# Performance work log

Measured on AMD Instinct MI355X. Metric: run time of the kernel, lower is better.

Reference implementation:

```python
import jax, jax.numpy as jnp
import numpy as np


def setup_inputs() -> dict:
    key = jax.random.key(0)
    k1, k2 = jax.random.split(key)
    N, D, G = 200000, 256, 512
    x = jax.random.normal(k1, (N, D), dtype=jnp.float32)
    batch_ids = jnp.sort(jax.random.randint(k2, (N,), 0, G, dtype=jnp.int64))
    return {"x": x, "batch_ids": batch_ids, "num_graphs": G}


def reference(x, batch_ids, num_graphs):
    # Segment-mean: equivalent to the per-graph masked mean loop.
    sums = jax.ops.segment_sum(x, batch_ids, num_segments=num_graphs)  # [G, D]
    counts = jax.ops.segment_sum(jnp.ones((x.shape[0],), dtype=x.dtype),
                                 batch_ids, num_segments=num_graphs)  # [G]
    graph_features = sums / counts[:, None]
    return graph_features
```

## Files before the change

kernel.cpp:

```cpp
#include <hip/hip_runtime.h>


#define SPLIT 4

__global__ __launch_bounds__(256) void segmean_partial(
    const float* __restrict__ x,
    const int*   __restrict__ ids,
    float*       __restrict__ part,
    int*         __restrict__ cnts,
    int N, int D, int G)
{
    const int bid = (int)blockIdx.x;
    const int g   = bid >> 2;
    const int q   = bid & 3;

    const int W  = 4096;
    const int v0 = g, v1 = g + 1;
    const long long c0 = (long long)v0 * N / G;
    const long long c1 = (long long)v1 * N / G;
    int lo0 = (int)(c0 - W < 0 ? 0 : c0 - W);
    int hi0 = (int)(c0 + W > N ? N : c0 + W);
    int lo1 = (int)(c1 - W < 0 ? 0 : c1 - W);
    int hi1 = (int)(c1 + W > N ? N : c1 + W);
    const bool ok0 = (lo0 == 0 || ids[lo0 - 1] < v0) && (hi0 == N || ids[hi0] >= v0);
    const bool ok1 = (lo1 == 0 || ids[lo1 - 1] < v1) && (hi1 == N || ids[hi1] >= v1);
    if (!ok0) { lo0 = 0; hi0 = N; }
    if (!ok1) { lo1 = 0; hi1 = N; }
    while ((lo0 < hi0) | (lo1 < hi1)) {
        if (lo0 < hi0) {
            const int m = (lo0 + hi0) >> 1;
            if (ids[m] < v0) lo0 = m + 1; else hi0 = m;
        }
        if (lo1 < hi1) {
            const int m = (lo1 + hi1) >> 1;
            if (ids[m] < v1) lo1 = m + 1; else hi1 = m;
        }
    }
    const int start = lo0, end = lo1;
    const int count = end - start;

    const int chunk = (count + SPLIT - 1) >> 2;
    const int r0 = start + q * chunk;
    const int r1 = (r0 + chunk < end) ? (r0 + chunk) : end;

    const int t      = (int)threadIdx.x;
    const int rowoff = t >> 6;
    const int col    = (t & 63) << 2;

    float4 acc = make_float4(0.f, 0.f, 0.f, 0.f);
    #pragma unroll 4
    for (int r = r0 + rowoff; r < r1; r += 4) {
        const float4 v = *reinterpret_cast<const float4*>(x + (size_t)r * (size_t)D + col);
        acc.x += v.x; acc.y += v.y; acc.z += v.z; acc.w += v.w;
    }

    __shared__ float4 sd[256];
    sd[t] = acc;
    __syncthreads();

    if (t < 64) {
        const float4 a = sd[t];
        const float4 b = sd[t + 64];
        const float4 c = sd[t + 128];
        const float4 d = sd[t + 192];
        float4 s;
        s.x = (a.x + b.x) + (c.x + d.x);
        s.y = (a.y + b.y) + (c.y + d.y);
        s.z = (a.z + b.z) + (c.z + d.z);
        s.w = (a.w + b.w) + (c.w + d.w);
        *reinterpret_cast<float4*>(part + (size_t)bid * (size_t)D + col) = s;
    }
    if (q == 0 && t == 0) cnts[g] = count;
}

__global__ __launch_bounds__(256) void segmean_combine(
    const float* __restrict__ part,
    const int*   __restrict__ cnts,
    float*       __restrict__ out,
    int D)
{
    const int g = (int)blockIdx.x;
    const float inv = 1.0f / (float)cnts[g];
    const float* p = part + (size_t)g * SPLIT * (size_t)D;
    for (int d = (int)threadIdx.x; d < D; d += (int)blockDim.x) {
        const float s = (p[d] + p[d + D]) + (p[d + 2 * D] + p[d + 3 * D]);
        out[(size_t)g * (size_t)D + d] = s * inv;
    }
}

extern "C" void kernel_launch(void* const* d_in, const int* in_sizes, int n_in,
                              void* d_out, int out_size, void* d_ws, size_t ws_size,
                              hipStream_t stream) {
    const float* x   = (const float*)d_in[0];
    const int*   ids = (const int*)d_in[1];
    float*       out = (float*)d_out;

    const int N = in_sizes[1];
    const int D = in_sizes[0] / N;
    const int G = out_size / D;

    float* part = (float*)d_ws;
    int*   cnts = (int*)((char*)d_ws + (size_t)G * SPLIT * D * sizeof(float));

    segmean_partial<<<dim3(G * SPLIT), dim3(256), 0, stream>>>(x, ids, part, cnts, N, D, G);
    segmean_combine<<<dim3(G), dim3(256), 0, stream>>>(part, cnts, out, D);
}
```

Measured before the change: 43.38 us.

## Fuse partial and combine into one 1024-thread block per segment

Replaces the two-kernel split (4 blocks per graph plus a combine kernel) with a single kernel using one 1024-thread block per graph, which reduces the segment in shared memory and writes the mean directly. This removes the second launch and the workspace round trip, and the binary search now runs once per graph instead of four times. Loads use nontemporal hints. In exchange there are only 512 blocks, and their larger size may lower occupancy flexibility. The shared-memory tree reduction also adds several syncthreads.

```diff
diff --git a/kernel.cpp b/kernel.cpp
--- a/kernel.cpp
+++ b/kernel.cpp
@@ -1,18 +1,15 @@
 #include <hip/hip_runtime.h>
 
 
-#define SPLIT 4
+typedef float f32x4 __attribute__((ext_vector_type(4)));
 
-__global__ __launch_bounds__(256) void segmean_partial(
+__global__ __launch_bounds__(1024) void segmean_kernel(
     const float* __restrict__ x,
     const int*   __restrict__ ids,
-    float*       __restrict__ part,
-    int*         __restrict__ cnts,
+    float*       __restrict__ out,
     int N, int D, int G)
 {
-    const int bid = (int)blockIdx.x;
-    const int g   = bid >> 2;
-    const int q   = bid & 3;
+    const int g = (int)blockIdx.x;
 
     const int W  = 4096;
     const int v0 = g, v1 = g + 1;
@@ -39,52 +36,32 @@
     const int start = lo0, end = lo1;
     const int count = end - start;
 
-    const int chunk = (count + SPLIT - 1) >> 2;
-    const int r0 = start + q * chunk;
-    const int r1 = (r0 + chunk < end) ? (r0 + chunk) : end;
-
     const int t      = (int)threadIdx.x;
     const int rowoff = t >> 6;
     const int col    = (t & 63) << 2;
 
-    float4 acc = make_float4(0.f, 0.f, 0.f, 0.f);
+    f32x4 acc = (f32x4)(0.f);
     #pragma unroll 4
-    for (int r = r0 + rowoff; r < r1; r += 4) {
-        const float4 v = *reinterpret_cast<const float4*>(x + (size_t)r * (size_t)D + col);
-        acc.x += v.x; acc.y += v.y; acc.z += v.z; acc.w += v.w;
+    for (int r = start + rowoff; r < end; r += 16) {
+        const f32x4 v = __builtin_nontemporal_load(
+            reinterpret_cast<const f32x4*>(x + (size_t)r * (size_t)D + col));
+        acc += v;
     }
 
-    __shared__ float4 sd[256];
+    __shared__ f32x4 sd[1024];
     sd[t] = acc;
     __syncthreads();
-
+    if (t < 512) sd[t] += sd[t + 512];
+    __syncthreads();
+    if (t < 256) sd[t] += sd[t + 256];
+    __syncthreads();
+    if (t < 128) sd[t] += sd[t + 128];
+    __syncthreads();
     if (t < 64) {
-        const float4 a = sd[t];
-        const float4 b = sd[t + 64];
-        const float4 c = sd[t + 128];
-        const float4 d = sd[t + 192];
-        float4 s;
-        s.x = (a.x + b.x) + (c.x + d.x);
-        s.y = (a.y + b.y) + (c.y + d.y);
-        s.z = (a.z + b.z) + (c.z + d.z);
-        s.w = (a.w + b.w) + (c.w + d.w);
-        *reinterpret_cast<float4*>(part + (size_t)bid * (size_t)D + col) = s;
-    }
-    if (q == 0 && t == 0) cnts[g] = count;
-}
-
-__global__ __launch_bounds__(256) void segmean_combine(
-    const float* __restrict__ part,
-    const int*   __restrict__ cnts,
-    float*       __restrict__ out,
-    int D)
-{
-    const int g = (int)blockIdx.x;
-    const float inv = 1.0f / (float)cnts[g];
-    const float* p = part + (size_t)g * SPLIT * (size_t)D;
-    for (int d = (int)threadIdx.x; d < D; d += (int)blockDim.x) {
-        const float s = (p[d] + p[d + D]) + (p[d + 2 * D] + p[d + 3 * D]);
-        out[(size_t)g * (size_t)D + d] = s * inv;
+        const f32x4 s = sd[t] + sd[t + 64];
+        const float inv = 1.0f / (float)count;
+        const f32x4 o = s * inv;
+        *reinterpret_cast<f32x4*>(out + (size_t)g * (size_t)D + col) = o;
     }
 }
 
@@ -99,9 +76,5 @@
     const int D = in_sizes[0] / N;
     const int G = out_size / D;
 
-    float* part = (float*)d_ws;
-    int*   cnts = (int*)((char*)d_ws + (size_t)G * SPLIT * D * sizeof(float));
-
-    segmean_partial<<<dim3(G * SPLIT), dim3(256), 0, stream>>>(x, ids, part, cnts, N, D, G);
-    segmean_combine<<<dim3(G), dim3(256), 0, stream>>>(part, cnts, out, D);
+    segmean_kernel<<<dim3(G), dim3(1024), 0, stream>>>(x, ids, out, N, D, G);
 }
```

Result: faster. 38.18 us (-12.0%).
